# Kernel tuning notes

Hardware: AMD Instinct MI355X
Metric: run time of the kernel (lower is better)

The kernel has to match this reference:

```python
import jax, jax.numpy as jnp
import numpy as np

B, S, E = 4, 2048, 1024
H, DK, DV = 16, 64, 128


def setup_inputs() -> dict:
    key = jax.random.key(0)
    ks = jax.random.split(key, 9)
    scale = 0.02
    x = jax.random.normal(ks[0], (B, S, E), dtype=jnp.float32)
    # Per-head linear weights stacked along a head axis (same math as the
    # torch ModuleList of nn.Linear(embed_dim, d) layers).
    Wq = jax.random.normal(ks[1], (H, E, DK), dtype=jnp.float32) * scale
    bq = jax.random.normal(ks[2], (H, DK), dtype=jnp.float32) * scale
    Wk = jax.random.normal(ks[3], (H, E, DK), dtype=jnp.float32) * scale
    bk = jax.random.normal(ks[4], (H, DK), dtype=jnp.float32) * scale
    Wv = jax.random.normal(ks[5], (H, E, DV), dtype=jnp.float32) * scale
    bv = jax.random.normal(ks[6], (H, DV), dtype=jnp.float32) * scale
    Wo = jax.random.normal(ks[7], (H * DV, E), dtype=jnp.float32) * scale
    bo = jax.random.normal(ks[8], (E,), dtype=jnp.float32) * scale
    return {"x": x, "Wq": Wq, "bq": bq, "Wk": Wk, "bk": bk,
            "Wv": Wv, "bv": bv, "Wo": Wo, "bo": bo}


def reference(x, Wq, bq, Wk, bk, Wv, bv, Wo, bo):
    # Batched equivalent of the per-head Linear loop: [B,S,E] x [H,E,D] -> [B,H,S,D]
    Q = jnp.einsum('bse,hed->bhsd', x, Wq) + bq[None, :, None, :]
    K = jnp.einsum('bse,hed->bhsd', x, Wk) + bk[None, :, None, :]
    V = jnp.einsum('bse,hed->bhsd', x, Wv) + bv[None, :, None, :]
    scale = 1.0 / jnp.sqrt(jnp.asarray(Q.shape[-1], dtype=Q.dtype))
    scores = jnp.einsum('bhqd,bhkd->bhqk', Q, K) * scale  # [B,H,S,S]
    causal_mask = jnp.triu(jnp.ones((S, S), dtype=bool), k=1)  # True above diagonal
    scores = jnp.where(causal_mask[None, None], jnp.asarray(-jnp.inf, scores.dtype), scores)
    probs = jax.nn.softmax(scores, axis=-1)
    attn = jnp.einsum('bhqk,bhkd->bhqd', probs, V)  # [B,H,S,DV]
    # transpose(1,2).view(B,S,H*DV)
    concat = attn.transpose(0, 2, 1, 3).reshape(x.shape[0], x.shape[1], -1)
    return concat @ Wo + bo
```

## Files before the change

kernel.cpp:

```cpp
#include <hip/hip_runtime.h>

typedef __bf16 bf16x8 __attribute__((ext_vector_type(8)));
typedef float f32x4 __attribute__((ext_vector_type(4)));
typedef float f32x16 __attribute__((ext_vector_type(16)));

static constexpr int Bb = 4, Ss = 2048, Ee = 1024, Hh = 16, DKk = 64, DVv = 128;
static constexpr int Mm = Bb * Ss;
static constexpr int NQ = Hh * DKk;
static constexpr int NV = Hh * DVv;

#define MFMA16 __builtin_amdgcn_mfma_f32_16x16x32_bf16
#define MFMA32 __builtin_amdgcn_mfma_f32_32x32x16_bf16

#define GLL16(g, l) __builtin_amdgcn_global_load_lds(                        \
    (const __attribute__((address_space(1))) void*)(g),                      \
    (__attribute__((address_space(3))) void*)(l), 16, 0, 0)

#define SBAR()   asm volatile("s_barrier" ::: "memory")
#define WLGKM0() do { asm volatile("s_waitcnt lgkmcnt(0)" ::: "memory"); \
                      __builtin_amdgcn_sched_barrier(0); } while (0)
#define WVM(n)   asm volatile("s_waitcnt vmcnt(" #n ")" ::: "memory")

static __device__ __forceinline__ unsigned short f2b(float f) {
  unsigned int u = __float_as_uint(f);
  u += 0x7fffu + ((u >> 16) & 1u);
  return (unsigned short)(u >> 16);
}

__global__ __launch_bounds__(256) void cast_x_kernel(const float* __restrict__ in,
                                                     unsigned short* __restrict__ out, int n4) {
  int i = blockIdx.x * 256 + threadIdx.x;
  if (i >= n4) return;
  float4 v = reinterpret_cast<const float4*>(in)[i];
  ushort4 o;
  o.x = f2b(v.x); o.y = f2b(v.y); o.z = f2b(v.z); o.w = f2b(v.w);
  reinterpret_cast<ushort4*>(out)[i] = o;
}

__global__ __launch_bounds__(256) void transpose_cast_kernel(const float* __restrict__ in,
                                                             unsigned short* __restrict__ out,
                                                             int R, int C) {
  __shared__ float tile[32][33];
  int c0 = blockIdx.x * 32, r0 = blockIdx.y * 32;
  const float* ip = in + (size_t)blockIdx.z * R * C;
  unsigned short* op = out + (size_t)blockIdx.z * R * C;
  int tx = threadIdx.x, ty = threadIdx.y;
#pragma unroll
  for (int i = 0; i < 32; i += 8)
    tile[ty + i][tx] = ip[(size_t)(r0 + ty + i) * C + (c0 + tx)];
  __syncthreads();
#pragma unroll
  for (int i = 0; i < 32; i += 8)
    op[(size_t)(c0 + ty + i) * R + (r0 + tx)] = f2b(tile[tx][ty + i]);
}

template <int OUTMODE>
__global__ __launch_bounds__(512, 2) void gemm9_kernel(const unsigned short* __restrict__ A,
                                                       const unsigned short* __restrict__ BT,
                                                       const float* __restrict__ bias1,
                                                       const float* __restrict__ bias2,
                                                       void* __restrict__ out1,
                                                       void* __restrict__ out2,
                                                       int N, int K) {
  __shared__ unsigned short As0[256 * 64], As1[256 * 64];
  __shared__ unsigned short Bs0[256 * 64], Bs1[256 * 64];
  const int tid = threadIdx.x, wave = tid >> 6, lane = tid & 63;
  const int wm = wave >> 2, wn = wave & 3;
  const int l15 = lane & 15, lq = lane >> 4;
  const int nwg = gridDim.x, cpx = nwg >> 3;
  const int orig = (blockIdx.x & 7) * cpx + (blockIdx.x >> 3);
  const int bm = (orig & 31) << 8, bn = (orig >> 5) << 8;
  const int srow = tid >> 3;
  const int ssw = (((tid & 7) ^ (srow & 7)) << 3);
  const int rsw = l15 & 7;
  const int nIter = K >> 7;

  f32x4 acc[8][4] = {};
  bf16x8 bf[2][4];

#define LDA9(ASQ, MI, KK) \
  (*reinterpret_cast<const bf16x8*>(&(ASQ)[(size_t)((wm * 128 + (MI)*16 + l15) * 64) + (((((KK)*4 + lq)) ^ rsw) << 3)]))
#define LDB9(BSQ, NI, KK) \
  (*reinterpret_cast<const bf16x8*>(&(BSQ)[(size_t)((wn * 64 + (NI)*16 + l15) * 64) + (((((KK)*4 + lq)) ^ rsw) << 3)]))

  auto stA = [&](unsigned short* dst, int kt) {
#pragma unroll
    for (int k4 = 0; k4 < 4; ++k4)
      GLL16(A + (size_t)(bm + srow + k4 * 64) * K + kt * 64 + ssw,
            &dst[(size_t)(tid + k4 * 512) * 8]);
  };
  auto stB = [&](unsigned short* dst, int kt) {
#pragma unroll
    for (int k4 = 0; k4 < 4; ++k4)
      GLL16(BT + (size_t)(bn + srow + k4 * 64) * K + kt * 64 + ssw,
            &dst[(size_t)(tid + k4 * 512) * 8]);
  };

  stA(As0, 0);
  stB(Bs0, 0);
  stB(Bs1, 1);
  WVM(0);
  SBAR();

  for (int it = 0; it < nIter; ++it) {
    const bool notlast = (it < nIter - 1);
    {
      bf16x8 af[2][4];
#pragma unroll
      for (int kk = 0; kk < 2; ++kk)
#pragma unroll
        for (int m = 0; m < 4; ++m) af[kk][m] = LDA9(As0, m, kk);
#pragma unroll
      for (int kk = 0; kk < 2; ++kk)
#pragma unroll
        for (int ni = 0; ni < 4; ++ni) bf[kk][ni] = LDB9(Bs0, ni, kk);
      stA(As1, 2 * it + 1);
      SBAR();
      WLGKM0();
      __builtin_amdgcn_s_setprio(1);
#pragma unroll
      for (int kk = 0; kk < 2; ++kk)
#pragma unroll
        for (int m = 0; m < 4; ++m)
#pragma unroll
          for (int ni = 0; ni < 4; ++ni)
            acc[m][ni] = MFMA16(af[kk][m], bf[kk][ni], acc[m][ni], 0, 0, 0);
      __builtin_amdgcn_s_setprio(0);
      SBAR();
    }
    {
      bf16x8 af[2][4];
#pragma unroll
      for (int kk = 0; kk < 2; ++kk)
#pragma unroll
        for (int m = 0; m < 4; ++m) af[kk][m] = LDA9(As0, 4 + m, kk);
      if (notlast) stB(Bs0, 2 * it + 2);
      SBAR();
      WLGKM0();
      __builtin_amdgcn_s_setprio(1);
#pragma unroll
      for (int kk = 0; kk < 2; ++kk)
#pragma unroll
        for (int m = 0; m < 4; ++m)
#pragma unroll
          for (int ni = 0; ni < 4; ++ni)
            acc[4 + m][ni] = MFMA16(af[kk][m], bf[kk][ni], acc[4 + m][ni], 0, 0, 0);
      __builtin_amdgcn_s_setprio(0);
      if (notlast) { WVM(4); } else { WVM(0); }
      SBAR();
    }
    {
      bf16x8 af[2][4];
#pragma unroll
      for (int kk = 0; kk < 2; ++kk)
#pragma unroll
        for (int m = 0; m < 4; ++m) af[kk][m] = LDA9(As1, m, kk);
#pragma unroll
      for (int kk = 0; kk < 2; ++kk)
#pragma unroll
        for (int ni = 0; ni < 4; ++ni) bf[kk][ni] = LDB9(Bs1, ni, kk);
      if (notlast) stA(As0, 2 * it + 2);
      SBAR();
      WLGKM0();
      __builtin_amdgcn_s_setprio(1);
#pragma unroll
      for (int kk = 0; kk < 2; ++kk)
#pragma unroll
        for (int m = 0; m < 4; ++m)
#pragma unroll
          for (int ni = 0; ni < 4; ++ni)
            acc[m][ni] = MFMA16(af[kk][m], bf[kk][ni], acc[m][ni], 0, 0, 0);
      __builtin_amdgcn_s_setprio(0);
      SBAR();
    }
    {
      bf16x8 af[2][4];
#pragma unroll
      for (int kk = 0; kk < 2; ++kk)
#pragma unroll
        for (int m = 0; m < 4; ++m) af[kk][m] = LDA9(As1, 4 + m, kk);
      if (notlast) stB(Bs1, 2 * it + 3);
      SBAR();
      WLGKM0();
      __builtin_amdgcn_s_setprio(1);
#pragma unroll
      for (int kk = 0; kk < 2; ++kk)
#pragma unroll
        for (int m = 0; m < 4; ++m)
#pragma unroll
          for (int ni = 0; ni < 4; ++ni)
            acc[4 + m][ni] = MFMA16(af[kk][m], bf[kk][ni], acc[4 + m][ni], 0, 0, 0);
      __builtin_amdgcn_s_setprio(0);
      if (notlast) WVM(4);
      SBAR();
    }
  }

  const float SCLQ = 0.125f * 1.44269504088896f;
#pragma unroll
  for (int ni = 0; ni < 4; ++ni) {
    int col = bn + wn * 64 + ni * 16 + l15;
    float bs;
    if (OUTMODE == 4)
      bs = (col < 1024) ? bias1[col] : bias2[col - 1024];
    else
      bs = bias1[col];
#pragma unroll
    for (int mi = 0; mi < 8; ++mi) {
      int row0 = bm + wm * 128 + mi * 16 + (lq << 2);
      if (OUTMODE == 2) {
        int b_ = row0 >> 11, s0 = row0 & 2047;
        unsigned short* dst = (unsigned short*)out1 +
            ((size_t)((b_ * Hh + (col >> 7)) * DVv + (col & 127))) * Ss + s0;
        ushort4 o;
        o.x = f2b(acc[mi][ni][0] + bs);
        o.y = f2b(acc[mi][ni][1] + bs);
        o.z = f2b(acc[mi][ni][2] + bs);
        o.w = f2b(acc[mi][ni][3] + bs);
        *reinterpret_cast<ushort4*>(dst) = o;
      } else {
        unsigned short* tgt = (unsigned short*)(col < 1024 ? out1 : out2);
        int cc = col & 1023, hh = cc >> 6, d = cc & 63;
#pragma unroll
        for (int r = 0; r < 4; ++r) {
          int row = row0 + r;
          int b_ = row >> 11, s0 = row & 2047;
          float v = acc[mi][ni][r] + bs;
          if (col < 1024) v *= SCLQ;
          tgt[(((size_t)(b_ * Hh + hh) * Ss + s0) << 6) + d] = f2b(v);
        }
      }
    }
  }
#undef LDA9
#undef LDB9
}

__global__ __launch_bounds__(512, 2) void gemm8f_kernel(const unsigned short* __restrict__ A,
                                                        const unsigned short* __restrict__ BT,
                                                        const float* __restrict__ bias1,
                                                        float* __restrict__ out1,
                                                        int N, int K) {
  __shared__ unsigned short As0[256 * 64], As1[256 * 64];
  __shared__ unsigned short Bs0[128 * 64], Bs1[128 * 64];
  const int tid = threadIdx.x, wave = tid >> 6, lane = tid & 63;
  const int wm = wave >> 1, wn = wave & 1;
  const int l15 = lane & 15, lq = lane >> 4;
  const int nwg = gridDim.x, cpx = nwg >> 3;
  const int orig = (blockIdx.x & 7) * cpx + (blockIdx.x >> 3);
  const int bm = (orig & 31) << 8, bn = (orig >> 5) << 7;
  const int srow = tid >> 3;
  const int ssw = (((tid & 7) ^ (srow & 7)) << 3);
  const int rsw = l15 & 7;
  const int nIter = K >> 7;

  f32x4 acc[4][4] = {};
  bf16x8 bf[2][4];

#define LDA(ASQ, MI, KK) \
  (*reinterpret_cast<const bf16x8*>(&(ASQ)[(size_t)((wm * 64 + (MI)*16 + l15) * 64) + (((((KK)*4 + lq)) ^ rsw) << 3)]))
#define LDB(BSQ, NI, KK) \
  (*reinterpret_cast<const bf16x8*>(&(BSQ)[(size_t)((wn * 64 + (NI)*16 + l15) * 64) + (((((KK)*4 + lq)) ^ rsw) << 3)]))

  auto stA = [&](unsigned short* dst, int kt) {
#pragma unroll
    for (int k4 = 0; k4 < 4; ++k4)
      GLL16(A + (size_t)(bm + srow + k4 * 64) * K + kt * 64 + ssw,
            &dst[(size_t)(tid + k4 * 512) * 8]);
  };
  auto stB = [&](unsigned short* dst, int kt) {
#pragma unroll
    for (int k4 = 0; k4 < 2; ++k4)
      GLL16(BT + (size_t)(bn + srow + k4 * 64) * K + kt * 64 + ssw,
            &dst[(size_t)(tid + k4 * 512) * 8]);
  };

  stA(As0, 0);
  stB(Bs0, 0);
  stB(Bs1, 1);
  WVM(0);
  SBAR();

  for (int it = 0; it < nIter; ++it) {
    const bool notlast = (it < nIter - 1);
    {
      bf16x8 af[2][2];
      af[0][0] = LDA(As0, 0, 0); af[0][1] = LDA(As0, 1, 0);
      af[1][0] = LDA(As0, 0, 1); af[1][1] = LDA(As0, 1, 1);
#pragma unroll
      for (int kk = 0; kk < 2; ++kk)
#pragma unroll
        for (int ni = 0; ni < 4; ++ni) bf[kk][ni] = LDB(Bs0, ni, kk);
      stA(As1, 2 * it + 1);
      SBAR();
      WLGKM0();
      __builtin_amdgcn_s_setprio(1);
#pragma unroll
      for (int kk = 0; kk < 2; ++kk)
#pragma unroll
        for (int i = 0; i < 2; ++i)
#pragma unroll
          for (int ni = 0; ni < 4; ++ni)
            acc[i][ni] = MFMA16(af[kk][i], bf[kk][ni], acc[i][ni], 0, 0, 0);
      __builtin_amdgcn_s_setprio(0);
      SBAR();
    }
    {
      bf16x8 af[2][2];
      af[0][0] = LDA(As0, 2, 0); af[0][1] = LDA(As0, 3, 0);
      af[1][0] = LDA(As0, 2, 1); af[1][1] = LDA(As0, 3, 1);
      if (notlast) stB(Bs0, 2 * it + 2);
      SBAR();
      WLGKM0();
      __builtin_amdgcn_s_setprio(1);
#pragma unroll
      for (int kk = 0; kk < 2; ++kk)
#pragma unroll
        for (int i = 0; i < 2; ++i)
#pragma unroll
          for (int ni = 0; ni < 4; ++ni)
            acc[2 + i][ni] = MFMA16(af[kk][i], bf[kk][ni], acc[2 + i][ni], 0, 0, 0);
      __builtin_amdgcn_s_setprio(0);
      if (notlast) { WVM(2); } else { WVM(0); }
      SBAR();
    }
    {
      bf16x8 af[2][2];
      af[0][0] = LDA(As1, 0, 0); af[0][1] = LDA(As1, 1, 0);
      af[1][0] = LDA(As1, 0, 1); af[1][1] = LDA(As1, 1, 1);
#pragma unroll
      for (int kk = 0; kk < 2; ++kk)
#pragma unroll
        for (int ni = 0; ni < 4; ++ni) bf[kk][ni] = LDB(Bs1, ni, kk);
      if (notlast) stA(As0, 2 * it + 2);
      SBAR();
      WLGKM0();
      __builtin_amdgcn_s_setprio(1);
#pragma unroll
      for (int kk = 0; kk < 2; ++kk)
#pragma unroll
        for (int i = 0; i < 2; ++i)
#pragma unroll
          for (int ni = 0; ni < 4; ++ni)
            acc[i][ni] = MFMA16(af[kk][i], bf[kk][ni], acc[i][ni], 0, 0, 0);
      __builtin_amdgcn_s_setprio(0);
      SBAR();
    }
    {
      bf16x8 af[2][2];
      af[0][0] = LDA(As1, 2, 0); af[0][1] = LDA(As1, 3, 0);
      af[1][0] = LDA(As1, 2, 1); af[1][1] = LDA(As1, 3, 1);
      if (notlast) stB(Bs1, 2 * it + 3);
      SBAR();
      WLGKM0();
      __builtin_amdgcn_s_setprio(1);
#pragma unroll
      for (int kk = 0; kk < 2; ++kk)
#pragma unroll
        for (int i = 0; i < 2; ++i)
#pragma unroll
          for (int ni = 0; ni < 4; ++ni)
            acc[2 + i][ni] = MFMA16(af[kk][i], bf[kk][ni], acc[2 + i][ni], 0, 0, 0);
      __builtin_amdgcn_s_setprio(0);
      if (notlast) WVM(2);
      SBAR();
    }
  }

#pragma unroll
  for (int ni = 0; ni < 4; ++ni) {
    int col = bn + wn * 64 + ni * 16 + l15;
    float bs = bias1[col];
#pragma unroll
    for (int mi = 0; mi < 4; ++mi) {
      int row0 = bm + wm * 64 + mi * 16 + (lq << 2);
#pragma unroll
      for (int r = 0; r < 4; ++r)
        out1[(size_t)(row0 + r) * N + col] = acc[mi][ni][r] + bs;
    }
  }
#undef LDA
#undef LDB
}

__global__ __launch_bounds__(512, 1) void attn11_kernel(const unsigned short* __restrict__ Qh,
                                                        const unsigned short* __restrict__ Kh,
                                                        const unsigned short* __restrict__ Vt,
                                                        unsigned short* __restrict__ Aw) {
  __shared__ unsigned short Kb[2][64 * 64];
  __shared__ unsigned short Vb[2][128 * 64];
  const int bid = blockIdx.x;
  const int phase = bid >> 8, idx = bid & 255;
  const int xcd = idx & 7, sub = idx >> 3;
  const int bhL = sub >> 2, q = sub & 3;
  const int bh = xcd + (bhL << 3);
  const int b = bh >> 4, h = bh & 15;
  const int qt = phase ? q : 7 - q;
  const int tid = threadIdx.x, wave = tid >> 6, lane = tid & 63;
  const int l31 = lane & 31, lh = lane >> 5;

  const unsigned short* Qsrc = Qh + (size_t)(b * Hh + h) * Ss * DKk;
  const unsigned short* Ksrc = Kh + (size_t)(b * Hh + h) * Ss * DKk;
  const unsigned short* Vsrc = Vt + (size_t)(b * Hh + h) * (size_t)DVv * Ss;
  unsigned short* Adst = Aw + (size_t)b * Ss * NV + h * DVv;

  const int nt = (qt + 1) * 4;
  const int q0w = qt * 256 + wave * 32;

  const int srow = tid >> 3, sch = tid & 7;
  const int soff = ((sch ^ (srow & 7)) << 3);
  const int rx = l31 & 7;

  union PU { unsigned u[4]; bf16x8 v; };

  bf16x8 qf[4];
#pragma unroll
  for (int ks = 0; ks < 4; ++ks)
    qf[ks] = *reinterpret_cast<const bf16x8*>(
        Qsrc + (size_t)(q0w + l31) * DKk + ks * 16 + lh * 8);

  f32x16 accO[4] = {};
  float mrow = -1e30f, lrow = 0.f;

  {
    GLL16(Ksrc + (size_t)srow * DKk + soff, &Kb[0][(size_t)tid * 8]);
    GLL16(Vsrc + (size_t)srow * Ss + soff, &Vb[0][(size_t)tid * 8]);
    GLL16(Vsrc + (size_t)(srow + 64) * Ss + soff, &Vb[0][(size_t)(tid + 512) * 8]);
  }

  for (int kt = 0; kt < nt; ++kt) {
    const int kbase = kt * 64;
    const int cur = kt & 1;
    __syncthreads();
    if (kt + 1 < nt) {
      const int nb = kbase + 64;
      const int nxt = cur ^ 1;
      GLL16(Ksrc + (size_t)(nb + srow) * DKk + soff, &Kb[nxt][(size_t)tid * 8]);
      GLL16(Vsrc + (size_t)srow * Ss + nb + soff, &Vb[nxt][(size_t)tid * 8]);
      GLL16(Vsrc + (size_t)(srow + 64) * Ss + nb + soff, &Vb[nxt][(size_t)(tid + 512) * 8]);
    }
    if (kbase > q0w + 31) continue;

    f32x16 accS[2] = {};
    __builtin_amdgcn_s_setprio(1);
#pragma unroll
    for (int kvb = 0; kvb < 2; ++kvb)
#pragma unroll
      for (int ks = 0; ks < 4; ++ks) {
        const unsigned short* kr = &Kb[cur][(kvb * 32 + l31) * 64];
        bf16x8 kf = *reinterpret_cast<const bf16x8*>(kr + (((ks * 2 + lh) ^ rx) << 3));
        accS[kvb] = MFMA32(kf, qf[ks], accS[kvb], 0, 0, 0);
      }
    __builtin_amdgcn_s_setprio(0);

    if (kbase + 63 > q0w) {
      int qg = q0w + l31;
#pragma unroll
      for (int kvb = 0; kvb < 2; ++kvb)
#pragma unroll
        for (int reg = 0; reg < 16; ++reg) {
          int kvg = kbase + kvb * 32 + (reg & 3) + 8 * (reg >> 2) + 4 * lh;
          if (kvg > qg) accS[kvb][reg] = -1e30f;
        }
    }
    float t[8];
#pragma unroll
    for (int i = 0; i < 8; ++i)
      t[i] = fmaxf(fmaxf(accS[0][i], accS[0][i + 8]), fmaxf(accS[1][i], accS[1][i + 8]));
    float pmx = fmaxf(fmaxf(fmaxf(t[0], t[1]), fmaxf(t[2], t[3])),
                      fmaxf(fmaxf(t[4], t[5]), fmaxf(t[6], t[7])));
    pmx = fmaxf(pmx, __shfl_xor(pmx, 32));
    float mn = mrow;
    if (!__all(pmx - mn <= 8.f)) {
      float mnew = fmaxf(mn, pmx);
      float al = exp2f(mn - mnew);
      mrow = mnew;
      lrow *= al;
#pragma unroll
      for (int reg = 0; reg < 16; ++reg) {
        float a = __shfl(al, (reg & 3) + 8 * (reg >> 2) + 4 * lh);
#pragma unroll
        for (int dvb = 0; dvb < 4; ++dvb) accO[dvb][reg] *= a;
      }
      mn = mnew;
    }
    float rs = 0.f;
#pragma unroll
    for (int kvb = 0; kvb < 2; ++kvb)
#pragma unroll
      for (int reg = 0; reg < 16; ++reg) {
        float e = exp2f(accS[kvb][reg] - mn);
        accS[kvb][reg] = e;
        rs += e;
      }
    rs += __shfl_xor(rs, 32);
    lrow += rs;
    bf16x8 pfrag[4];
#pragma unroll
    for (int kvb = 0; kvb < 2; ++kvb)
#pragma unroll
      for (int s = 0; s < 2; ++s) {
        const int B0 = s * 8;
        unsigned a, c, bb, d;
        asm("v_cvt_pk_bf16_f32 %0, %1, %2" : "=v"(a) : "v"(accS[kvb][B0 + 0]), "v"(accS[kvb][B0 + 1]));
        asm("v_cvt_pk_bf16_f32 %0, %1, %2" : "=v"(c) : "v"(accS[kvb][B0 + 2]), "v"(accS[kvb][B0 + 3]));
        asm("v_cvt_pk_bf16_f32 %0, %1, %2" : "=v"(bb) : "v"(accS[kvb][B0 + 4]), "v"(accS[kvb][B0 + 5]));
        asm("v_cvt_pk_bf16_f32 %0, %1, %2" : "=v"(d) : "v"(accS[kvb][B0 + 6]), "v"(accS[kvb][B0 + 7]));
        asm volatile("v_permlane32_swap_b32 %0, %1" : "+v"(a), "+v"(bb));
        asm volatile("v_permlane32_swap_b32 %0, %1" : "+v"(c), "+v"(d));
        PU u;
        u.u[0] = a; u.u[1] = c; u.u[2] = bb; u.u[3] = d;
        pfrag[kvb * 2 + s] = u.v;
      }
    __builtin_amdgcn_s_setprio(1);
#pragma unroll
    for (int dvb = 0; dvb < 4; ++dvb) {
      const unsigned short* vr = &Vb[cur][(dvb * 32 + l31) * 64];
#pragma unroll
      for (int ks = 0; ks < 4; ++ks) {
        bf16x8 vf = *reinterpret_cast<const bf16x8*>(vr + (((ks * 2 + lh) ^ rx) << 3));
        accO[dvb] = MFMA32(pfrag[ks], vf, accO[dvb], 0, 0, 0);
      }
    }
    __builtin_amdgcn_s_setprio(0);
  }
  float linv = 1.f / lrow;
#pragma unroll
  for (int reg = 0; reg < 16; ++reg) {
    int qr = (reg & 3) + 8 * (reg >> 2) + 4 * lh;
    float li = __shfl(linv, qr);
    int row = q0w + qr;
#pragma unroll
    for (int dvb = 0; dvb < 4; ++dvb)
      Adst[(size_t)row * NV + dvb * 32 + l31] = f2b(accO[dvb][reg] * li);
  }
}

extern "C" void kernel_launch(void* const* d_in, const int* in_sizes, int n_in,
                              void* d_out, int out_size, void* d_ws, size_t ws_size,
                              hipStream_t stream) {
  (void)in_sizes; (void)n_in; (void)out_size; (void)ws_size;
  const float* x  = (const float*)d_in[0];
  const float* Wq = (const float*)d_in[1];
  const float* bq = (const float*)d_in[2];
  const float* Wk = (const float*)d_in[3];
  const float* bk = (const float*)d_in[4];
  const float* Wv = (const float*)d_in[5];
  const float* bv = (const float*)d_in[6];
  const float* Wo = (const float*)d_in[7];
  const float* bo = (const float*)d_in[8];
  float* out = (float*)d_out;

  unsigned short* ws = (unsigned short*)d_ws;
  unsigned short* xb  = ws;
  unsigned short* WqT = xb  + 8388608;
  unsigned short* WkT = WqT + 1048576;
  unsigned short* WvT = WkT + 1048576;
  unsigned short* WoT = WvT + 2097152;
  unsigned short* Qw  = WoT + 2097152;
  unsigned short* Kw  = Qw  + 8388608;
  unsigned short* Vtw = Kw  + 8388608;
  unsigned short* Aw  = Vtw + 16777216;

  cast_x_kernel<<<dim3(8192), dim3(256), 0, stream>>>(x, xb, (Mm * Ee) / 4);

  transpose_cast_kernel<<<dim3(2, 32, 16), dim3(32, 8), 0, stream>>>(Wq, WqT, Ee, DKk);
  transpose_cast_kernel<<<dim3(2, 32, 16), dim3(32, 8), 0, stream>>>(Wk, WkT, Ee, DKk);
  transpose_cast_kernel<<<dim3(4, 32, 16), dim3(32, 8), 0, stream>>>(Wv, WvT, Ee, DVv);
  transpose_cast_kernel<<<dim3(32, 64, 1), dim3(32, 8), 0, stream>>>(Wo, WoT, NV, Ee);

  gemm9_kernel<4><<<dim3(256), dim3(512), 0, stream>>>(xb, WqT, bq, bk, Qw, Kw, 2048, Ee);
  gemm9_kernel<2><<<dim3(256), dim3(512), 0, stream>>>(xb, WvT, bv, nullptr, Vtw, nullptr, NV, Ee);

  attn11_kernel<<<dim3(512), dim3(512), 0, stream>>>(Qw, Kw, Vtw, Aw);

  gemm8f_kernel<<<dim3(256), dim3(512), 0, stream>>>(Aw, WoT, bo, out, NQ, NV);
}
```

Before: 282.4 us.

## Split attention into 128-row query tiles with 256-thread blocks and longest-first ordering

Changes the attention kernel from 512-thread blocks covering 256 query rows to 256-thread blocks covering 128 query rows, doubling the grid to 1024 blocks. Blocks are ordered so the longest causal tiles (highest qt) launch first, with heads grouped per XCD. The aim is better load balance and more concurrent blocks per CU, since launch bounds no longer force a single block per CU. The cost is that K/V tiles are loaded by more blocks, adding redundant global traffic, and each thread now issues more load instructions.

```diff
diff --git a/kernel.cpp b/kernel.cpp
--- a/kernel.cpp
+++ b/kernel.cpp
@@ -383,19 +383,18 @@
 #undef LDB
 }
 
-__global__ __launch_bounds__(512, 1) void attn11_kernel(const unsigned short* __restrict__ Qh,
-                                                        const unsigned short* __restrict__ Kh,
-                                                        const unsigned short* __restrict__ Vt,
-                                                        unsigned short* __restrict__ Aw) {
+__global__ __launch_bounds__(256) void attn12_kernel(const unsigned short* __restrict__ Qh,
+                                                     const unsigned short* __restrict__ Kh,
+                                                     const unsigned short* __restrict__ Vt,
+                                                     unsigned short* __restrict__ Aw) {
   __shared__ unsigned short Kb[2][64 * 64];
   __shared__ unsigned short Vb[2][128 * 64];
   const int bid = blockIdx.x;
-  const int phase = bid >> 8, idx = bid & 255;
-  const int xcd = idx & 7, sub = idx >> 3;
-  const int bhL = sub >> 2, q = sub & 3;
-  const int bh = xcd + (bhL << 3);
+  const int xcd = bid & 7, rest = bid >> 3;
+  const int ord = rest >> 3, bhL = rest & 7;
+  const int bh = xcd * 8 + bhL;
   const int b = bh >> 4, h = bh & 15;
-  const int qt = phase ? q : 7 - q;
+  const int qt = 15 - ord;
   const int tid = threadIdx.x, wave = tid >> 6, lane = tid & 63;
   const int l31 = lane & 31, lh = lane >> 5;
 
@@ -404,8 +403,8 @@
   const unsigned short* Vsrc = Vt + (size_t)(b * Hh + h) * (size_t)DVv * Ss;
   unsigned short* Adst = Aw + (size_t)b * Ss * NV + h * DVv;
 
-  const int nt = (qt + 1) * 4;
-  const int q0w = qt * 256 + wave * 32;
+  const int nt = 2 * qt + 2;
+  const int q0w = qt * 128 + wave * 32;
 
   const int srow = tid >> 3, sch = tid & 7;
   const int soff = ((sch ^ (srow & 7)) << 3);
@@ -423,9 +422,12 @@
   float mrow = -1e30f, lrow = 0.f;
 
   {
-    GLL16(Ksrc + (size_t)srow * DKk + soff, &Kb[0][(size_t)tid * 8]);
-    GLL16(Vsrc + (size_t)srow * Ss + soff, &Vb[0][(size_t)tid * 8]);
-    GLL16(Vsrc + (size_t)(srow + 64) * Ss + soff, &Vb[0][(size_t)(tid + 512) * 8]);
+#pragma unroll
+    for (int k4 = 0; k4 < 2; ++k4)
+      GLL16(Ksrc + (size_t)(srow + k4 * 32) * DKk + soff, &Kb[0][(size_t)(tid + k4 * 256) * 8]);
+#pragma unroll
+    for (int k4 = 0; k4 < 4; ++k4)
+      GLL16(Vsrc + (size_t)(srow + k4 * 32) * Ss + soff, &Vb[0][(size_t)(tid + k4 * 256) * 8]);
   }
 
   for (int kt = 0; kt < nt; ++kt) {
@@ -435,9 +437,14 @@
     if (kt + 1 < nt) {
       const int nb = kbase + 64;
       const int nxt = cur ^ 1;
-      GLL16(Ksrc + (size_t)(nb + srow) * DKk + soff, &Kb[nxt][(size_t)tid * 8]);
-      GLL16(Vsrc + (size_t)srow * Ss + nb + soff, &Vb[nxt][(size_t)tid * 8]);
-      GLL16(Vsrc + (size_t)(srow + 64) * Ss + nb + soff, &Vb[nxt][(size_t)(tid + 512) * 8]);
+#pragma unroll
+      for (int k4 = 0; k4 < 2; ++k4)
+        GLL16(Ksrc + (size_t)(nb + srow + k4 * 32) * DKk + soff,
+              &Kb[nxt][(size_t)(tid + k4 * 256) * 8]);
+#pragma unroll
+      for (int k4 = 0; k4 < 4; ++k4)
+        GLL16(Vsrc + (size_t)(srow + k4 * 32) * Ss + nb + soff,
+              &Vb[nxt][(size_t)(tid + k4 * 256) * 8]);
     }
     if (kbase > q0w + 31) continue;
 
@@ -572,7 +579,7 @@
   gemm9_kernel<4><<<dim3(256), dim3(512), 0, stream>>>(xb, WqT, bq, bk, Qw, Kw, 2048, Ee);
   gemm9_kernel<2><<<dim3(256), dim3(512), 0, stream>>>(xb, WvT, bv, nullptr, Vtw, nullptr, NV, Ee);
 
-  attn11_kernel<<<dim3(512), dim3(512), 0, stream>>>(Qw, Kw, Vtw, Aw);
+  attn12_kernel<<<dim3(1024), dim3(256), 0, stream>>>(Qw, Kw, Vtw, Aw);
 
   gemm8f_kernel<<<dim3(256), dim3(512), 0, stream>>>(Aw, WoT, bo, out, NQ, NV);
 }
```

Result: slower. 303.6 us (+7.5%).

## Pair causal q-tiles per block and stage 128-row KV tiles

Applied to the files above, without the earlier changes.

The attention kernel now launches 256 blocks, and each block handles two query tiles in sequence (a long one and its complementary short one). This balances causal work inside a block instead of relying on the scheduler. KV tiles grow to 128 keys per stage, with a wider XOR swizzle on V, so there are half as many barriers and load batches per key range. The cost is doubled LDS use (about 96KB) and a serial second phase per block with no overlap between the two phases.

```diff
diff --git a/kernel.cpp b/kernel.cpp
--- a/kernel.cpp
+++ b/kernel.cpp
@@ -383,19 +383,17 @@
 #undef LDB
 }
 
-__global__ __launch_bounds__(512, 1) void attn11_kernel(const unsigned short* __restrict__ Qh,
+__global__ __launch_bounds__(512, 1) void attn14_kernel(const unsigned short* __restrict__ Qh,
                                                         const unsigned short* __restrict__ Kh,
                                                         const unsigned short* __restrict__ Vt,
                                                         unsigned short* __restrict__ Aw) {
-  __shared__ unsigned short Kb[2][64 * 64];
-  __shared__ unsigned short Vb[2][128 * 64];
+  __shared__ unsigned short Kb[2][128 * 64];
+  __shared__ unsigned short Vb[2][128 * 128];
   const int bid = blockIdx.x;
-  const int phase = bid >> 8, idx = bid & 255;
-  const int xcd = idx & 7, sub = idx >> 3;
-  const int bhL = sub >> 2, q = sub & 3;
+  const int xcd = bid & 7, sub_ = bid >> 3;
+  const int bhL = sub_ >> 2, q = sub_ & 3;
   const int bh = xcd + (bhL << 3);
   const int b = bh >> 4, h = bh & 15;
-  const int qt = phase ? q : 7 - q;
   const int tid = threadIdx.x, wave = tid >> 6, lane = tid & 63;
   const int l31 = lane & 31, lh = lane >> 5;
 
@@ -404,135 +402,165 @@
   const unsigned short* Vsrc = Vt + (size_t)(b * Hh + h) * (size_t)DVv * Ss;
   unsigned short* Adst = Aw + (size_t)b * Ss * NV + h * DVv;
 
-  const int nt = (qt + 1) * 4;
-  const int q0w = qt * 256 + wave * 32;
-
-  const int srow = tid >> 3, sch = tid & 7;
-  const int soff = ((sch ^ (srow & 7)) << 3);
+  const int srowK = tid >> 3, schK = tid & 7;
+  const int srowV = tid >> 4, schV = tid & 15;
   const int rx = l31 & 7;
+  const int rxv = l31 & 15;
 
   union PU { unsigned u[4]; bf16x8 v; };
 
-  bf16x8 qf[4];
-#pragma unroll
-  for (int ks = 0; ks < 4; ++ks)
-    qf[ks] = *reinterpret_cast<const bf16x8*>(
-        Qsrc + (size_t)(q0w + l31) * DKk + ks * 16 + lh * 8);
-
-  f32x16 accO[4] = {};
-  float mrow = -1e30f, lrow = 0.f;
-
-  {
-    GLL16(Ksrc + (size_t)srow * DKk + soff, &Kb[0][(size_t)tid * 8]);
-    GLL16(Vsrc + (size_t)srow * Ss + soff, &Vb[0][(size_t)tid * 8]);
-    GLL16(Vsrc + (size_t)(srow + 64) * Ss + soff, &Vb[0][(size_t)(tid + 512) * 8]);
-  }
-
-  for (int kt = 0; kt < nt; ++kt) {
-    const int kbase = kt * 64;
-    const int cur = kt & 1;
+#pragma unroll 1
+  for (int ph = 0; ph < 2; ++ph) {
+    const int qt = ph ? q : 7 - q;
+    const int nt2 = (qt + 1) * 2;
+    const int q0w = qt * 256 + wave * 32;
+
+    bf16x8 qf[4];
+#pragma unroll
+    for (int ks = 0; ks < 4; ++ks)
+      qf[ks] = *reinterpret_cast<const bf16x8*>(
+          Qsrc + (size_t)(q0w + l31) * DKk + ks * 16 + lh * 8);
+
+    f32x16 accO[4] = {};
+    float mrow = -1e30f, lrow = 0.f;
+
+    {
+#pragma unroll
+      for (int k4 = 0; k4 < 2; ++k4) {
+        int kvr = srowK + k4 * 64;
+        GLL16(Ksrc + (size_t)kvr * DKk + ((schK ^ (kvr & 7)) << 3),
+              &Kb[0][(size_t)(tid + k4 * 512) * 8]);
+      }
+#pragma unroll
+      for (int k4 = 0; k4 < 4; ++k4) {
+        int dvr = srowV + k4 * 32;
+        GLL16(Vsrc + (size_t)dvr * Ss + ((schV ^ (dvr & 15)) << 3),
+              &Vb[0][(size_t)(tid + k4 * 512) * 8]);
+      }
+    }
+
+    for (int T = 0; T < nt2; ++T) {
+      const int cur = T & 1;
+      __syncthreads();
+      if (T + 1 < nt2) {
+        const int nb2 = (T + 1) * 128;
+        const int nxt = cur ^ 1;
+#pragma unroll
+        for (int k4 = 0; k4 < 2; ++k4) {
+          int kvr = srowK + k4 * 64;
+          GLL16(Ksrc + (size_t)(nb2 + kvr) * DKk + ((schK ^ (kvr & 7)) << 3),
+                &Kb[nxt][(size_t)(tid + k4 * 512) * 8]);
+        }
+#pragma unroll
+        for (int k4 = 0; k4 < 4; ++k4) {
+          int dvr = srowV + k4 * 32;
+          GLL16(Vsrc + (size_t)dvr * Ss + nb2 + ((schV ^ (dvr & 15)) << 3),
+                &Vb[nxt][(size_t)(tid + k4 * 512) * 8]);
+        }
+      }
+#pragma unroll 1
+      for (int sub = 0; sub < 2; ++sub) {
+        const int kbase = T * 128 + sub * 64;
+        if (kbase > q0w + 31) continue;
+
+        f32x16 accS[2] = {};
+        __builtin_amdgcn_s_setprio(1);
+#pragma unroll
+        for (int kvb = 0; kvb < 2; ++kvb)
+#pragma unroll
+          for (int ks = 0; ks < 4; ++ks) {
+            const int row = sub * 64 + kvb * 32 + l31;
+            bf16x8 kf = *reinterpret_cast<const bf16x8*>(
+                &Kb[cur][row * 64 + (((ks * 2 + lh) ^ rx) << 3)]);
+            accS[kvb] = MFMA32(kf, qf[ks], accS[kvb], 0, 0, 0);
+          }
+        __builtin_amdgcn_s_setprio(0);
+
+        if (kbase + 63 > q0w) {
+          int qg = q0w + l31;
+#pragma unroll
+          for (int kvb = 0; kvb < 2; ++kvb)
+#pragma unroll
+            for (int reg = 0; reg < 16; ++reg) {
+              int kvg = kbase + kvb * 32 + (reg & 3) + 8 * (reg >> 2) + 4 * lh;
+              if (kvg > qg) accS[kvb][reg] = -1e30f;
+            }
+        }
+        float t[8];
+#pragma unroll
+        for (int i = 0; i < 8; ++i)
+          t[i] = fmaxf(fmaxf(accS[0][i], accS[0][i + 8]), fmaxf(accS[1][i], accS[1][i + 8]));
+        float pmx = fmaxf(fmaxf(fmaxf(t[0], t[1]), fmaxf(t[2], t[3])),
+                          fmaxf(fmaxf(t[4], t[5]), fmaxf(t[6], t[7])));
+        pmx = fmaxf(pmx, __shfl_xor(pmx, 32));
+        float mn = mrow;
+        if (!__all(pmx - mn <= 8.f)) {
+          float mnew = fmaxf(mn, pmx);
+          float al = exp2f(mn - mnew);
+          mrow = mnew;
+          lrow *= al;
+#pragma unroll
+          for (int reg = 0; reg < 16; ++reg) {
+            float a = __shfl(al, (reg & 3) + 8 * (reg >> 2) + 4 * lh);
+#pragma unroll
+            for (int dvb = 0; dvb < 4; ++dvb) accO[dvb][reg] *= a;
+          }
+          mn = mnew;
+        }
+        float rs = 0.f;
+#pragma unroll
+        for (int kvb = 0; kvb < 2; ++kvb)
+#pragma unroll
+          for (int reg = 0; reg < 16; ++reg) {
+            float e = exp2f(accS[kvb][reg] - mn);
+            accS[kvb][reg] = e;
+            rs += e;
+          }
+        rs += __shfl_xor(rs, 32);
+        lrow += rs;
+        bf16x8 pfrag[4];
+#pragma unroll
+        for (int kvb = 0; kvb < 2; ++kvb)
+#pragma unroll
+          for (int s = 0; s < 2; ++s) {
+            const int B0 = s * 8;
+            unsigned a, c, bb, d;
+            asm("v_cvt_pk_bf16_f32 %0, %1, %2" : "=v"(a) : "v"(accS[kvb][B0 + 0]), "v"(accS[kvb][B0 + 1]));
+            asm("v_cvt_pk_bf16_f32 %0, %1, %2" : "=v"(c) : "v"(accS[kvb][B0 + 2]), "v"(accS[kvb][B0 + 3]));
+            asm("v_cvt_pk_bf16_f32 %0, %1, %2" : "=v"(bb) : "v"(accS[kvb][B0 + 4]), "v"(accS[kvb][B0 + 5]));
+            asm("v_cvt_pk_bf16_f32 %0, %1, %2" : "=v"(d) : "v"(accS[kvb][B0 + 6]), "v"(accS[kvb][B0 + 7]));
+            asm volatile("v_permlane32_swap_b32 %0, %1" : "+v"(a), "+v"(bb));
+            asm volatile("v_permlane32_swap_b32 %0, %1" : "+v"(c), "+v"(d));
+            PU u;
+            u.u[0] = a; u.u[1] = c; u.u[2] = bb; u.u[3] = d;
+            pfrag[kvb * 2 + s] = u.v;
+          }
+        __builtin_amdgcn_s_setprio(1);
+#pragma unroll
+        for (int dvb = 0; dvb < 4; ++dvb) {
+          const int dv = dvb * 32 + l31;
+          const unsigned short* vr = &Vb[cur][dv * 128];
+#pragma unroll
+          for (int ks = 0; ks < 4; ++ks) {
+            bf16x8 vf = *reinterpret_cast<const bf16x8*>(
+                vr + ((((sub << 3) + ks * 2 + lh) ^ rxv) << 3));
+            accO[dvb] = MFMA32(pfrag[ks], vf, accO[dvb], 0, 0, 0);
+          }
+        }
+        __builtin_amdgcn_s_setprio(0);
+      }
+    }
+    float linv = 1.f / lrow;
+#pragma unroll
+    for (int reg = 0; reg < 16; ++reg) {
+      int qr = (reg & 3) + 8 * (reg >> 2) + 4 * lh;
+      float li = __shfl(linv, qr);
+      int row = q0w + qr;
+#pragma unroll
+      for (int dvb = 0; dvb < 4; ++dvb)
+        Adst[(size_t)row * NV + dvb * 32 + l31] = f2b(accO[dvb][reg] * li);
+    }
     __syncthreads();
-    if (kt + 1 < nt) {
-      const int nb = kbase + 64;
-      const int nxt = cur ^ 1;
-      GLL16(Ksrc + (size_t)(nb + srow) * DKk + soff, &Kb[nxt][(size_t)tid * 8]);
-      GLL16(Vsrc + (size_t)srow * Ss + nb + soff, &Vb[nxt][(size_t)tid * 8]);
-      GLL16(Vsrc + (size_t)(srow + 64) * Ss + nb + soff, &Vb[nxt][(size_t)(tid + 512) * 8]);
-    }
-    if (kbase > q0w + 31) continue;
-
-    f32x16 accS[2] = {};
-    __builtin_amdgcn_s_setprio(1);
-#pragma unroll
-    for (int kvb = 0; kvb < 2; ++kvb)
-#pragma unroll
-      for (int ks = 0; ks < 4; ++ks) {
-        const unsigned short* kr = &Kb[cur][(kvb * 32 + l31) * 64];
-        bf16x8 kf = *reinterpret_cast<const bf16x8*>(kr + (((ks * 2 + lh) ^ rx) << 3));
-        accS[kvb] = MFMA32(kf, qf[ks], accS[kvb], 0, 0, 0);
-      }
-    __builtin_amdgcn_s_setprio(0);
-
-    if (kbase + 63 > q0w) {
-      int qg = q0w + l31;
-#pragma unroll
-      for (int kvb = 0; kvb < 2; ++kvb)
-#pragma unroll
-        for (int reg = 0; reg < 16; ++reg) {
-          int kvg = kbase + kvb * 32 + (reg & 3) + 8 * (reg >> 2) + 4 * lh;
-          if (kvg > qg) accS[kvb][reg] = -1e30f;
-        }
-    }
-    float t[8];
-#pragma unroll
-    for (int i = 0; i < 8; ++i)
-      t[i] = fmaxf(fmaxf(accS[0][i], accS[0][i + 8]), fmaxf(accS[1][i], accS[1][i + 8]));
-    float pmx = fmaxf(fmaxf(fmaxf(t[0], t[1]), fmaxf(t[2], t[3])),
-                      fmaxf(fmaxf(t[4], t[5]), fmaxf(t[6], t[7])));
-    pmx = fmaxf(pmx, __shfl_xor(pmx, 32));
-    float mn = mrow;
-    if (!__all(pmx - mn <= 8.f)) {
-      float mnew = fmaxf(mn, pmx);
-      float al = exp2f(mn - mnew);
-      mrow = mnew;
-      lrow *= al;
-#pragma unroll
-      for (int reg = 0; reg < 16; ++reg) {
-        float a = __shfl(al, (reg & 3) + 8 * (reg >> 2) + 4 * lh);
-#pragma unroll
-        for (int dvb = 0; dvb < 4; ++dvb) accO[dvb][reg] *= a;
-      }
-      mn = mnew;
-    }
-    float rs = 0.f;
-#pragma unroll
-    for (int kvb = 0; kvb < 2; ++kvb)
-#pragma unroll
-      for (int reg = 0; reg < 16; ++reg) {
-        float e = exp2f(accS[kvb][reg] - mn);
-        accS[kvb][reg] = e;
-        rs += e;
-      }
-    rs += __shfl_xor(rs, 32);
-    lrow += rs;
-    bf16x8 pfrag[4];
-#pragma unroll
-    for (int kvb = 0; kvb < 2; ++kvb)
-#pragma unroll
-      for (int s = 0; s < 2; ++s) {
-        const int B0 = s * 8;
-        unsigned a, c, bb, d;
-        asm("v_cvt_pk_bf16_f32 %0, %1, %2" : "=v"(a) : "v"(accS[kvb][B0 + 0]), "v"(accS[kvb][B0 + 1]));
-        asm("v_cvt_pk_bf16_f32 %0, %1, %2" : "=v"(c) : "v"(accS[kvb][B0 + 2]), "v"(accS[kvb][B0 + 3]));
-        asm("v_cvt_pk_bf16_f32 %0, %1, %2" : "=v"(bb) : "v"(accS[kvb][B0 + 4]), "v"(accS[kvb][B0 + 5]));
-        asm("v_cvt_pk_bf16_f32 %0, %1, %2" : "=v"(d) : "v"(accS[kvb][B0 + 6]), "v"(accS[kvb][B0 + 7]));
-        asm volatile("v_permlane32_swap_b32 %0, %1" : "+v"(a), "+v"(bb));
-        asm volatile("v_permlane32_swap_b32 %0, %1" : "+v"(c), "+v"(d));
-        PU u;
-        u.u[0] = a; u.u[1] = c; u.u[2] = bb; u.u[3] = d;
-        pfrag[kvb * 2 + s] = u.v;
-      }
-    __builtin_amdgcn_s_setprio(1);
-#pragma unroll
-    for (int dvb = 0; dvb < 4; ++dvb) {
-      const unsigned short* vr = &Vb[cur][(dvb * 32 + l31) * 64];
-#pragma unroll
-      for (int ks = 0; ks < 4; ++ks) {
-        bf16x8 vf = *reinterpret_cast<const bf16x8*>(vr + (((ks * 2 + lh) ^ rx) << 3));
-        accO[dvb] = MFMA32(pfrag[ks], vf, accO[dvb], 0, 0, 0);
-      }
-    }
-    __builtin_amdgcn_s_setprio(0);
-  }
-  float linv = 1.f / lrow;
-#pragma unroll
-  for (int reg = 0; reg < 16; ++reg) {
-    int qr = (reg & 3) + 8 * (reg >> 2) + 4 * lh;
-    float li = __shfl(linv, qr);
-    int row = q0w + qr;
-#pragma unroll
-    for (int dvb = 0; dvb < 4; ++dvb)
-      Adst[(size_t)row * NV + dvb * 32 + l31] = f2b(accO[dvb][reg] * li);
   }
 }
 
@@ -572,7 +600,7 @@
   gemm9_kernel<4><<<dim3(256), dim3(512), 0, stream>>>(xb, WqT, bq, bk, Qw, Kw, 2048, Ee);
   gemm9_kernel<2><<<dim3(256), dim3(512), 0, stream>>>(xb, WvT, bv, nullptr, Vtw, nullptr, NV, Ee);
 
-  attn11_kernel<<<dim3(512), dim3(512), 0, stream>>>(Qw, Kw, Vtw, Aw);
+  attn14_kernel<<<dim3(256), dim3(512), 0, stream>>>(Qw, Kw, Vtw, Aw);
 
   gemm8f_kernel<<<dim3(256), dim3(512), 0, stream>>>(Aw, WoT, bo, out, NQ, NV);
 }
```

Result: faster. 246.6 us (-12.7%).
